# Kernel optimization log

Hardware: AMD Instinct MI355X
Metric: run time of the kernel (lower is better)

## Reference

```python
import jax, jax.numpy as jnp
import numpy as np

FEAT_STRIDE = 8
IM_DIMS = (4096.0, 4096.0)  # (height, width)
ANCHOR_SCALES = (8.0, 16.0, 32.0)
RATIOS = (0.5, 1.0, 2.0)
PRE_NMS_TOPN = 12000   # TRAIN cfg (eval_mode=False)
POST_NMS_TOPN = 2000
NMS_THRESH = 0.7
MIN_SIZE = 16.0


def _generate_anchors(base_size=16.0, ratios=RATIOS, scales=ANCHOR_SCALES):
    ratios = np.array(ratios, np.float32)
    scales = np.array(scales, np.float32)
    w = h = float(base_size)
    x_ctr = 0.5 * (w - 1.0)
    y_ctr = 0.5 * (h - 1.0)
    size = w * h
    ws = np.round(np.sqrt(size / ratios))
    hs = np.round(ws * ratios)
    out = []
    for wr, hr in zip(ws, hs):
        wss = wr * scales
        hss = hr * scales
        out.append(np.stack([x_ctr - 0.5 * (wss - 1.0), y_ctr - 0.5 * (hss - 1.0),
                             x_ctr + 0.5 * (wss - 1.0), y_ctr + 0.5 * (hss - 1.0)], axis=1))
    return np.concatenate(out, 0).astype(np.float32)  # [A=9, 4]


def _nms(boxes, scores, thresh, max_out):
    # greedy sequential NMS; indices are discrete -> stop gradients here
    boxes = jax.lax.stop_gradient(boxes)
    scores = jax.lax.stop_gradient(scores)
    areas = (boxes[:, 2] - boxes[:, 0] + 1.0) * (boxes[:, 3] - boxes[:, 1] + 1.0)

    def body(i, state):
        supp, keep = state
        idx = jnp.argmax(jnp.where(supp, -jnp.inf, scores))
        b = boxes[idx]
        xx1 = jnp.maximum(b[0], boxes[:, 0])
        yy1 = jnp.maximum(b[1], boxes[:, 1])
        xx2 = jnp.minimum(b[2], boxes[:, 2])
        yy2 = jnp.minimum(b[3], boxes[:, 3])
        inter = jnp.maximum(0.0, xx2 - xx1 + 1.0) * jnp.maximum(0.0, yy2 - yy1 + 1.0)
        iou = inter / (areas[idx] + areas - inter)
        supp = supp | (iou > thresh)  # also suppresses idx itself (iou==1)
        keep = keep.at[i].set(idx.astype(jnp.int32))
        return supp, keep

    supp0 = jnp.zeros(boxes.shape[0], dtype=bool)
    keep0 = jnp.zeros(max_out, dtype=jnp.int32)
    _, keep = jax.lax.fori_loop(0, max_out, body, (supp0, keep0))
    return keep


def reference(rpn_cls_score, rpn_bbox_pred):
    _, H, W, C2 = rpn_cls_score.shape
    A = C2 // 2
    # rpn_softmax: per-anchor 2-way (bg, fg) softmax; channels laid out [2, A]
    prob = jax.nn.softmax(rpn_cls_score.reshape(H, W, 2, A), axis=2)
    scores = prob[:, :, 1, :].reshape(-1)           # fg scores, [H*W*A]
    deltas = rpn_bbox_pred.reshape(-1, 4)           # [H*W*A, 4]

    # anchors shifted over the feature grid
    anchors = jnp.asarray(_generate_anchors())       # [A, 4]
    sx = jnp.arange(W, dtype=jnp.float32) * FEAT_STRIDE
    sy = jnp.arange(H, dtype=jnp.float32) * FEAT_STRIDE
    shift_x, shift_y = jnp.meshgrid(sx, sy)          # [H, W]
    shifts = jnp.stack([shift_x, shift_y, shift_x, shift_y], -1).reshape(-1, 1, 4)
    all_anchors = (anchors[None, :, :] + shifts).reshape(-1, 4)  # [H*W*A, 4]

    # bbox_transform_inv
    ws = all_anchors[:, 2] - all_anchors[:, 0] + 1.0
    hs = all_anchors[:, 3] - all_anchors[:, 1] + 1.0
    cx = all_anchors[:, 0] + 0.5 * ws
    cy = all_anchors[:, 1] + 0.5 * hs
    dx, dy, dw, dh = deltas[:, 0], deltas[:, 1], deltas[:, 2], deltas[:, 3]
    pcx = dx * ws + cx
    pcy = dy * hs + cy
    pw = jnp.exp(dw) * ws
    ph = jnp.exp(dh) * hs
    x1 = pcx - 0.5 * pw
    y1 = pcy - 0.5 * ph
    x2 = pcx + 0.5 * pw
    y2 = pcy + 0.5 * ph

    # clip to image boundaries
    x1 = jnp.clip(x1, 0.0, IM_DIMS[1] - 1.0)
    y1 = jnp.clip(y1, 0.0, IM_DIMS[0] - 1.0)
    x2 = jnp.clip(x2, 0.0, IM_DIMS[1] - 1.0)
    y2 = jnp.clip(y2, 0.0, IM_DIMS[0] - 1.0)
    proposals = jnp.stack([x1, y1, x2, y2], axis=1)

    # drop tiny boxes (jit-friendly: -inf score instead of physical removal)
    keep_min = ((x2 - x1 + 1.0) >= MIN_SIZE) & ((y2 - y1 + 1.0) >= MIN_SIZE)
    scores = jnp.where(keep_min, scores, -jnp.inf)

    top_scores, order = jax.lax.top_k(scores, PRE_NMS_TOPN)
    props = proposals[order]                         # [pre_nms_topN, 4]
    keep = _nms(props, top_scores, NMS_THRESH, POST_NMS_TOPN)
    rois = props[keep]                               # [post_nms_topN, 4]
    # blob: [batch_idx(=0), x1, y1, x2, y2]
    return jnp.concatenate([jnp.zeros((POST_NMS_TOPN, 1), rois.dtype), rois], axis=1)


def setup_inputs() -> dict:
    key = jax.random.key(0)
    k1, k2 = jax.random.split(key)
    rpn_cls_score = jax.random.normal(k1, (1, 512, 512, 18), dtype=jnp.float32)
    rpn_bbox_pred = jax.random.normal(k2, (1, 512, 512, 36), dtype=jnp.float32) * 0.2
    return {"rpn_cls_score": rpn_cls_score, "rpn_bbox_pred": rpn_bbox_pred}
```

## Files before the change

kernel.cpp:

```cpp
#include <hip/hip_runtime.h>
#include <cstdint>
#include <cstddef>

#pragma clang fp contract(off)

#define N_ANCH 2359296
#define K_PRE  12000
#define K_POST 2000
#define NWORD  188
#define NC     94
#define TIE_CAP 65536

typedef unsigned int u32;
typedef unsigned long long u64;

__constant__ float c_anch[9][4] = {
  { -84.f,  -40.f,   99.f,   55.f },
  { -176.f, -88.f,  191.f,  103.f },
  { -360.f, -184.f, 375.f,  199.f },
  { -56.f,  -56.f,   71.f,   71.f },
  { -120.f, -120.f, 135.f,  135.f },
  { -248.f, -248.f, 263.f,  263.f },
  { -36.f,  -80.f,   51.f,   95.f },
  { -80.f,  -168.f,  95.f,  183.f },
  { -168.f, -344.f, 183.f,  359.f },
};

__device__ __forceinline__ float pexpf(float xin) {
#pragma clang fp contract(off)
  const float exp_hi = 88.3762626647950f;
  const float exp_lo = -88.3762626647949f;
  const float LOG2EF = 1.44269504088896341f;
  const float C1 = 0.693359375f;
  const float C2 = -2.12194440e-4f;
  const float p0 = 1.9875691500E-4f;
  const float p1 = 1.3981999507E-3f;
  const float p2 = 8.3334519073E-3f;
  const float p3 = 4.1665795894E-2f;
  const float p4 = 1.6666665459E-1f;
  const float p5 = 5.0000001201E-1f;
  float x = fminf(fmaxf(xin, exp_lo), exp_hi);
  float fx = floorf(x * LOG2EF + 0.5f);
  float tmp = C1 * fx;
  float z = C2 * fx;
  x = x - tmp;
  x = x - z;
  z = x * x;
  float y = x * p0 + p1;
  y = y * x + p2;
  y = y * x + p3;
  y = y * x + p4;
  y = y * x + p5;
  y = y * z + x;
  y = 1.0f + y;
  int n = (int)fx;
  u32 e = ((u32)(n + 127)) << 23;
  return y * __uint_as_float(e);
}

__device__ __forceinline__ void decode_box(const float* __restrict__ bbox, int aidx,
                                           float4* ob, float* oarea, bool* okeep) {
#pragma clang fp contract(off)
  int pos = aidx / 9;
  int a = aidx - pos * 9;
  int w = pos & 511;
  int h = pos >> 9;
  float shx = (float)(w * 8);
  float shy = (float)(h * 8);
  float ax1 = c_anch[a][0] + shx;
  float ay1 = c_anch[a][1] + shy;
  float ax2 = c_anch[a][2] + shx;
  float ay2 = c_anch[a][3] + shy;
  float aw = (ax2 - ax1) + 1.0f;
  float ah = (ay2 - ay1) + 1.0f;
  float acx = ax1 + 0.5f * aw;
  float acy = ay1 + 0.5f * ah;
  const float* d = bbox + (size_t)pos * 36 + (size_t)a * 4;
  float dx = d[0], dy = d[1], dw = d[2], dh = d[3];
  float pcx = dx * aw + acx;
  float pcy = dy * ah + acy;
  float pw = pexpf(dw) * aw;
  float ph = pexpf(dh) * ah;
  float x1 = pcx - 0.5f * pw;
  float y1 = pcy - 0.5f * ph;
  float x2 = pcx + 0.5f * pw;
  float y2 = pcy + 0.5f * ph;
  x1 = fminf(fmaxf(x1, 0.0f), 4095.0f);
  y1 = fminf(fmaxf(y1, 0.0f), 4095.0f);
  x2 = fminf(fmaxf(x2, 0.0f), 4095.0f);
  y2 = fminf(fmaxf(y2, 0.0f), 4095.0f);
  *ob = make_float4(x1, y1, x2, y2);
  float ww = (x2 - x1) + 1.0f;
  float hh = (y2 - y1) + 1.0f;
  *oarea = ww * hh;
  *okeep = (ww >= 16.0f) && (hh >= 16.0f);
}

__global__ void k_scores(const float* __restrict__ cls, const float* __restrict__ bbox,
                         u32* __restrict__ keys, u32* __restrict__ ctl,
                         u32* __restrict__ hist) {
#pragma clang fp contract(off)
  int t = blockIdx.x * blockDim.x + threadIdx.x;
  if (blockIdx.x == 0) {
    if (threadIdx.x < 16) ctl[threadIdx.x] = (threadIdx.x == 1) ? (u32)K_PRE : 0u;
    hist[threadIdx.x] = 0u;
  }
  if (t >= N_ANCH) return;
  int pos = t / 9;
  int a = t - pos * 9;
  float s0 = cls[(size_t)pos * 18 + a];
  float s1 = cls[(size_t)pos * 18 + 9 + a];
  float m = fmaxf(s0, s1);
  float e0 = pexpf(s0 - m);
  float e1 = pexpf(s1 - m);
  float p = e1 / (e0 + e1);
  float4 box; float area; bool km;
  decode_box(bbox, t, &box, &area, &km);
  keys[t] = km ? (__float_as_uint(p) | 0x80000000u) : 0u;
}

__global__ void k_histscan(const u32* __restrict__ keys, u32* __restrict__ ctl,
                           u32* __restrict__ hist, int shift, int pass) {
  __shared__ u32 lh[4][256];
  __shared__ u32 s_last;
  int t = threadIdx.x;
  lh[0][t] = 0u; lh[1][t] = 0u; lh[2][t] = 0u; lh[3][t] = 0u;
  __syncthreads();
  int sub = t & 3;
  u32 prefix = ctl[0];
  u32 msk = (shift == 24) ? 0u : (0xFFFFFFFFu << (shift + 8));
  int stride = gridDim.x * blockDim.x;
  for (int i = blockIdx.x * blockDim.x + t; i < N_ANCH; i += stride) {
    u32 k = keys[i];
    if ((k & msk) == prefix) atomicAdd(&lh[sub][(k >> shift) & 0xFFu], 1u);
  }
  __syncthreads();
  u32 hsum = lh[0][t] + lh[1][t] + lh[2][t] + lh[3][t];
  if (hsum) atomicAdd(&hist[t], hsum);
  __syncthreads();
  if (t == 0) {
    __threadfence();
    u32 old = atomicAdd(&ctl[8 + pass], 1u);
    s_last = (old == gridDim.x - 1) ? 1u : 0u;
  }
  __syncthreads();
  if (!s_last) return;
  __threadfence();
  __shared__ u32 sh[256];
  __shared__ u32 horig[256];
  __shared__ int s_d;
  u32 h = atomicAdd(&hist[t], 0u);
  sh[t] = h; horig[t] = h;
  if (t == 0) s_d = 0;
  u32 krem = ctl[1];
  __syncthreads();
  u32 v = h;
  for (int off = 1; off < 256; off <<= 1) {
    u32 add = (t + off < 256) ? sh[t + off] : 0u;
    __syncthreads();
    v += add;
    sh[t] = v;
    __syncthreads();
  }
  if (sh[t] >= krem) atomicMax(&s_d, t);
  __syncthreads();
  if (t == 0) {
    int d = s_d;
    u32 cum = sh[d] - horig[d];
    ctl[0] |= ((u32)d) << shift;
    ctl[1] = krem - cum;
    if (shift == 0) { ctl[2] = ctl[0]; ctl[3] = ctl[1]; }
  }
  hist[t] = 0u;
}

__global__ void k_collect(const u32* __restrict__ keys, u32* __restrict__ ctl,
                          int* __restrict__ sel, int* __restrict__ tie,
                          u64* __restrict__ comps) {
  __shared__ int stI[2048];
  __shared__ u64 stC[2048];
  __shared__ int stT[256];
  __shared__ u32 s_cnt, s_tcnt, s_base, s_tbase;
  int tid = threadIdx.x;
  if (tid == 0) { s_cnt = 0; s_tcnt = 0; }
  __syncthreads();
  u32 kstar = ctl[2];
  int stride = gridDim.x * blockDim.x;
  for (int i = blockIdx.x * blockDim.x + tid; i < N_ANCH; i += stride) {
    u32 k = keys[i];
    if (k > kstar) {
      u32 p = atomicAdd(&s_cnt, 1u);
      u64 cmp = ((u64)k << 32) | (u64)(0xFFFFFFFFu - (u32)i);
      if (p < 2048u) { stI[p] = i; stC[p] = cmp; }
      else { u32 g = atomicAdd(&ctl[4], 1u); sel[g] = i; comps[g] = cmp; }
    } else if (k == kstar) {
      u32 p = atomicAdd(&s_tcnt, 1u);
      if (p < 256u) stT[p] = i;
      else { u32 g = atomicAdd(&ctl[5], 1u); if (g < TIE_CAP) tie[g] = i; }
    }
  }
  __syncthreads();
  if (tid == 0) {
    u32 n = min(s_cnt, 2048u);
    s_base = atomicAdd(&ctl[4], n);
    u32 tn = min(s_tcnt, 256u);
    s_tbase = atomicAdd(&ctl[5], tn);
  }
  __syncthreads();
  u32 n = min(s_cnt, 2048u);
  for (u32 q = tid; q < n; q += blockDim.x) {
    sel[s_base + q] = stI[q];
    comps[s_base + q] = stC[q];
  }
  u32 tn = min(s_tcnt, 256u);
  for (u32 q = tid; q < tn; q += blockDim.x) {
    u32 g = s_tbase + q;
    if (g < TIE_CAP) tie[g] = stT[q];
  }
}

__global__ void k_tiepick(const u32* __restrict__ ctl, const int* __restrict__ tie,
                          int* __restrict__ sel, u64* __restrict__ comps) {
  u32 T = ctl[5]; if (T > TIE_CAP) T = TIE_CAP;
  if (T > 8192u) T = 8192u;
  u32 need = ctl[3];
  u32 base = ctl[4];
  u32 kstar = ctl[2];
  for (u32 t = threadIdx.x; t < T; t += blockDim.x) {
    int v = tie[t];
    u32 r = 0;
    for (u32 u = 0; u < T; ++u) r += (tie[u] < v) ? 1u : 0u;
    if (r < need) {
      sel[base + r] = v;
      comps[base + r] = ((u64)kstar << 32) | (u64)(0xFFFFFFFFu - (u32)v);
    }
  }
}

__global__ void k_rankdec(const u64* __restrict__ comps, const int* __restrict__ sel,
                          const float* __restrict__ bbox,
                          float4* __restrict__ props, float* __restrict__ areas) {
  __shared__ u64 tile[2048];
  int tid = threadIdx.x;
  int lane = tid & 63;
  int wave = tid >> 6;
  int base = (blockIdx.x * 4 + wave) * 8;
  u64 c0 = comps[base + 0], c1 = comps[base + 1], c2 = comps[base + 2], c3 = comps[base + 3];
  u64 c4 = comps[base + 4], c5 = comps[base + 5], c6 = comps[base + 6], c7 = comps[base + 7];
  int n0 = 0, n1 = 0, n2 = 0, n3 = 0, n4 = 0, n5 = 0, n6 = 0, n7 = 0;
  for (int t0 = 0; t0 < K_PRE; t0 += 2048) {
    int cnt = min(2048, K_PRE - t0);
    __syncthreads();
    for (int q = tid; q < cnt; q += 256) tile[q] = comps[t0 + q];
    __syncthreads();
    for (int q = lane; q < cnt; q += 64) {
      u64 v = tile[q];
      n0 += (v > c0); n1 += (v > c1); n2 += (v > c2); n3 += (v > c3);
      n4 += (v > c4); n5 += (v > c5); n6 += (v > c6); n7 += (v > c7);
    }
  }
  for (int off = 32; off; off >>= 1) {
    n0 += __shfl_xor(n0, off); n1 += __shfl_xor(n1, off);
    n2 += __shfl_xor(n2, off); n3 += __shfl_xor(n3, off);
    n4 += __shfl_xor(n4, off); n5 += __shfl_xor(n5, off);
    n6 += __shfl_xor(n6, off); n7 += __shfl_xor(n7, off);
  }
  int rk = n0;
  rk = (lane == 1) ? n1 : rk; rk = (lane == 2) ? n2 : rk;
  rk = (lane == 3) ? n3 : rk; rk = (lane == 4) ? n4 : rk;
  rk = (lane == 5) ? n5 : rk; rk = (lane == 6) ? n6 : rk;
  rk = (lane == 7) ? n7 : rk;
  if (lane < 8) {
    float4 box; float area; bool km;
    decode_box(bbox, sel[base + lane], &box, &area, &km);
    props[rk] = box;
    areas[rk] = area;
  }
}

__device__ __forceinline__ int d2idx(int c, int h, int lane) {
  return ((c * 2 + h) * 64 + lane) * 2;
}

__global__ void k_mask(const float4* __restrict__ props, const float* __restrict__ areas,
                       u64* __restrict__ mask, u64* __restrict__ diag2,
                       u64* __restrict__ sub2) {
#pragma clang fp contract(off)
  int x = blockIdx.x, y = blockIdx.y;
  int cx = x >> 1, cy = y >> 1;
  if (cy + 1 < cx || cy == cx + 1) return;
  __shared__ float4 bj[64];
  __shared__ float aj[64];
  int j0 = y * 64;
  bj[threadIdx.x] = props[j0 + threadIdx.x];
  aj[threadIdx.x] = areas[j0 + threadIdx.x];
  __syncthreads();
  int i = x * 64 + threadIdx.x;
  float4 bi = props[i];
  float ai = areas[i];
  u64 bits = 0;
  for (int jj = 0; jj < 64; ++jj) {
    int j = j0 + jj;
    float4 bb = bj[jj];
    float xx1 = fmaxf(bi.x, bb.x);
    float yy1 = fmaxf(bi.y, bb.y);
    float xx2 = fminf(bi.z, bb.z);
    float yy2 = fminf(bi.w, bb.w);
    float w = fmaxf(0.0f, (xx2 - xx1) + 1.0f);
    float h = fmaxf(0.0f, (yy2 - yy1) + 1.0f);
    float inter = w * h;
    float iou = inter / ((ai + aj[jj]) - inter);
    if ((iou > 0.7f) && (j < K_PRE)) bits |= (1ull << jj);
  }
  if (cy == cx)          diag2[d2idx(cx, x & 1, threadIdx.x) + (y & 1)] = bits;
  else if (cy == cx - 1) sub2[d2idx(cx, x & 1, threadIdx.x) + (y & 1)] = bits;
  else                   mask[(size_t)i * NWORD + y] = bits;
}

#define NMS_BAR() asm volatile("s_waitcnt lgkmcnt(0)\n\ts_barrier" ::: "memory")

typedef __attribute__((address_space(1))) const u32* gas_p;
typedef __attribute__((address_space(3))) u32* las_p;
__device__ __forceinline__ void gll16(const u64* g, u64* l) {
  __builtin_amdgcn_global_load_lds((gas_p)g, (las_p)l, 16, 0, 0);
}

__global__ void __launch_bounds__(1024, 1) k_nms(const u64* __restrict__ mask,
                                                 const u64* __restrict__ diag2,
                                                 const u64* __restrict__ sub2,
                                                 const float4* __restrict__ props,
                                                 float* __restrict__ out) {
  __shared__ u64 rem[NWORD];
  __shared__ int keepb[K_POST];
  __shared__ int kept[2][128];
  __shared__ u64 dstage[2][2][64][2];
  __shared__ u64 sstage[2][2][64][2];
  __shared__ int s_kk[2];
  __shared__ int s_nk;
  __shared__ int s_brk;
  int tid = threadIdx.x;
  int lane = tid & 63;
  int wave = tid >> 6;
  for (int w = tid; w < NWORD; w += 1024) {
    int base = w * 64;
    u64 v;
    if (base + 64 <= K_PRE) v = 0ull;
    else if (base >= K_PRE) v = ~0ull;
    else v = (~0ull) << (K_PRE - base);
    rem[w] = v;
  }
  if (tid == 0) { s_nk = 0; s_brk = 0; s_kk[0] = 0; s_kk[1] = 0; }
  if (wave == 0) {
    gll16(diag2 + d2idx(0, 0, lane), &dstage[0][0][0][0]);
    gll16(diag2 + d2idx(0, 1, lane), &dstage[0][1][0][0]);
    gll16(sub2 + d2idx(1, 0, lane), &sstage[1][0][0][0]);
    gll16(sub2 + d2idx(1, 1, lane), &sstage[1][1][0][0]);
  }
  __syncthreads();

  int nk = 0;

  for (int c = 0; c < NC; ++c) {
    if (s_brk) break;
    int par = c & 1;
    if (wave == 0) {
      int cn = min(c + 1, NC - 1);
      int cs = min(c + 2, NC - 1);
      gll16(diag2 + d2idx(cn, 0, lane), &dstage[cn & 1][0][0][0]);
      gll16(diag2 + d2idx(cn, 1, lane), &dstage[cn & 1][1][0][0]);
      gll16(sub2 + d2idx(cs, 0, lane), &sstage[cs & 1][0][0][0]);
      gll16(sub2 + d2idx(cs, 1, lane), &sstage[cs & 1][1][0][0]);
      asm volatile("s_waitcnt vmcnt(4)" ::: "memory");
      u64 dl0A = dstage[par][0][lane][0], dl1A = dstage[par][0][lane][1];
      u64 dh0A = dstage[par][1][lane][0], dh1A = dstage[par][1][lane][1];
      int ps = (c + 1) & 1;
      u64 sl0A = sstage[ps][0][lane][0], sl1A = sstage[ps][0][lane][1];
      u64 sh0A = sstage[ps][1][lane][0], sh1A = sstage[ps][1][lane][1];
      u64 w0 = ~rem[2 * c];
      u64 w1 = ~rem[2 * c + 1];
      u64 km0 = 0, km1 = 0;
      int nk0 = nk;
      while (w0 != 0ull && nk < K_POST) {
        int j = (int)__builtin_ctzll(w0);
        u64 sup = __ballot((int)((dl0A >> j) & 1ull));
        km0 |= (1ull << j);
        nk++;
        w0 &= ~sup;
      }
      if (km0) w1 &= ~__ballot((int)((dh0A & km0) != 0ull));
      while (w1 != 0ull && nk < K_POST) {
        int j = (int)__builtin_ctzll(w1);
        u64 sup = __ballot((int)((dh1A >> j) & 1ull));
        km1 |= (1ull << j);
        nk++;
        w1 &= ~sup;
      }
      int ncnt0 = __popcll(km0);
      u64 below = (1ull << lane) - 1ull;
      if ((km0 >> lane) & 1ull) {
        int pos = nk0 + __popcll(km0 & below);
        int idx = (c << 7) | lane;
        keepb[pos] = idx;
        kept[par][pos - nk0] = idx;
      }
      if ((km1 >> lane) & 1ull) {
        int pos = nk0 + ncnt0 + __popcll(km1 & below);
        int idx = (c << 7) | 64 | lane;
        keepb[pos] = idx;
        kept[par][pos - nk0] = idx;
      }
      if (c + 1 < NC) {
        int plo = (int)((((sl0A & km0) | (sl1A & km1)) != 0ull) ? 1 : 0);
        int phi = (int)((((sh0A & km0) | (sh1A & km1)) != 0ull) ? 1 : 0);
        u64 vlo = __ballot(plo);
        u64 vhi = __ballot(phi);
        if (lane == 0) {
          if (vlo) atomicOr((unsigned long long*)&rem[2 * c + 2], (unsigned long long)vlo);
          if (vhi) atomicOr((unsigned long long*)&rem[2 * c + 3], (unsigned long long)vhi);
        }
      }
      if (lane == 0) { s_kk[par] = nk - nk0; s_nk = nk; s_brk = (nk >= K_POST) ? 1 : 0; }
    } else if (c >= 1) {
      int kkp = s_kk[par ^ 1];
      const int* kb = &kept[par ^ 1][0];
      int wv = wave - 1;
      int seg = wv % 3;
      int q0 = wv / 3;
      int w = 2 * c + 2 + seg * 64 + lane;
      if (kkp > q0 && w < NWORD) {
        int m = kkp - 1;
        int i0 = kb[q0];
        int i1 = kb[min(q0 + 5, m)];
        int i2 = kb[min(q0 + 10, m)];
        int i3 = kb[min(q0 + 15, m)];
        int i4 = kb[min(q0 + 20, m)];
        int i5 = kb[min(q0 + 25, m)];
        int i6 = kb[min(q0 + 30, m)];
        int i7 = kb[min(q0 + 35, m)];
        u64 fp0 = mask[(size_t)i0 * NWORD + w];
        u64 fp1 = mask[(size_t)i1 * NWORD + w];
        u64 fp2 = mask[(size_t)i2 * NWORD + w];
        u64 fp3 = mask[(size_t)i3 * NWORD + w];
        u64 fp4 = mask[(size_t)i4 * NWORD + w];
        u64 fp5 = mask[(size_t)i5 * NWORD + w];
        u64 fp6 = mask[(size_t)i6 * NWORD + w];
        u64 fp7 = mask[(size_t)i7 * NWORD + w];
        u64 v = (fp0 | fp1) | (fp2 | fp3) | ((fp4 | fp5) | (fp6 | fp7));
        for (int q = q0 + 40; q < kkp; q += 5)
          v |= mask[(size_t)kb[q] * NWORD + w];
        if (v) atomicOr((unsigned long long*)&rem[w], (unsigned long long)v);
      }
    }
    NMS_BAR();
  }
  __syncthreads();
  int fnk = s_nk;
  for (int t = tid; t < K_POST; t += 1024) {
    int kidx = (t < fnk) ? keepb[t] : 0;
    float4 b = props[kidx];
    out[t * 5 + 0] = 0.0f;
    out[t * 5 + 1] = b.x;
    out[t * 5 + 2] = b.y;
    out[t * 5 + 3] = b.z;
    out[t * 5 + 4] = b.w;
  }
}

extern "C" void kernel_launch(void* const* d_in, const int* in_sizes, int n_in,
                              void* d_out, int out_size, void* d_ws, size_t ws_size,
                              hipStream_t stream) {
  const float* cls  = (const float*)d_in[0];
  const float* bbox = (const float*)d_in[1];
  float* out = (float*)d_out;
  char* ws = (char*)d_ws;

  u64* mask    = (u64*)ws;
  u32* keys    = (u32*)ws;
  u32* ctl     = (u32*)(ws + 9437184);
  u32* hist    = (u32*)(ws + 9437248);
  int* sel     = (int*)(ws + 9438464);
  int* tie     = (int*)(ws + 9486592);
  u64* comps   = (u64*)(ws + 18096128);
  float4* props= (float4*)(ws + 18240512);
  float* areas = (float*)(ws + 18433024);
  u64* diag2   = (u64*)(ws + 18481152);
  u64* sub2    = (u64*)(ws + 18673664);

  k_scores<<<dim3((N_ANCH + 255) / 256), dim3(256), 0, stream>>>(cls, bbox, keys, ctl, hist);
  const int shifts[4] = {24, 16, 8, 0};
  for (int s = 0; s < 4; ++s)
    k_histscan<<<dim3(256), dim3(256), 0, stream>>>(keys, ctl, hist, shifts[s], s);
  k_collect<<<dim3(256), dim3(256), 0, stream>>>(keys, ctl, sel, tie, comps);
  k_tiepick<<<dim3(1), dim3(256), 0, stream>>>(ctl, tie, sel, comps);
  k_rankdec<<<dim3(375), dim3(256), 0, stream>>>(comps, sel, bbox, props, areas);
  k_mask<<<dim3(188, 188), dim3(64), 0, stream>>>(props, areas, mask, diag2, sub2);
  k_nms<<<dim3(1), dim3(1024), 0, stream>>>(mask, diag2, sub2, props, out);
}
```

Measured before the change: 319.3 us.

## Widen histogram/collect blocks to 1024 threads and batch NMS mask loads via inline asm

The radix-select histogram and collect kernels now launch 1024-thread blocks instead of 256, with guards so that only the first 256 threads handle per-bin work. This adds more in-flight loads during the full scans over the keys. In the NMS kernel, the eight gathered mask loads are issued back-to-back in inline assembly with a single wait, forcing memory-level parallelism. The inline asm blocks compiler scheduling, and the shared staging buffers in k_collect may behave differently with four times the threads per block.

Result: faster. 304.8 us, median of 2 (-4.6%).

```diff
diff --git a/kernel.cpp b/kernel.cpp
--- a/kernel.cpp
+++ b/kernel.cpp
@@ -103,7 +103,7 @@
   int t = blockIdx.x * blockDim.x + threadIdx.x;
   if (blockIdx.x == 0) {
     if (threadIdx.x < 16) ctl[threadIdx.x] = (threadIdx.x == 1) ? (u32)K_PRE : 0u;
-    hist[threadIdx.x] = 0u;
+    if (threadIdx.x < 256) hist[threadIdx.x] = 0u;
   }
   if (t >= N_ANCH) return;
   int pos = t / 9;
@@ -119,12 +119,14 @@
   keys[t] = km ? (__float_as_uint(p) | 0x80000000u) : 0u;
 }
 
-__global__ void k_histscan(const u32* __restrict__ keys, u32* __restrict__ ctl,
-                           u32* __restrict__ hist, int shift, int pass) {
+__global__ void __launch_bounds__(1024) k_histscan(const u32* __restrict__ keys,
+                                                   u32* __restrict__ ctl,
+                                                   u32* __restrict__ hist,
+                                                   int shift, int pass) {
   __shared__ u32 lh[4][256];
   __shared__ u32 s_last;
   int t = threadIdx.x;
-  lh[0][t] = 0u; lh[1][t] = 0u; lh[2][t] = 0u; lh[3][t] = 0u;
+  if (t < 256) { lh[0][t] = 0u; lh[1][t] = 0u; lh[2][t] = 0u; lh[3][t] = 0u; }
   __syncthreads();
   int sub = t & 3;
   u32 prefix = ctl[0];
@@ -135,8 +137,10 @@
     if ((k & msk) == prefix) atomicAdd(&lh[sub][(k >> shift) & 0xFFu], 1u);
   }
   __syncthreads();
-  u32 hsum = lh[0][t] + lh[1][t] + lh[2][t] + lh[3][t];
-  if (hsum) atomicAdd(&hist[t], hsum);
+  if (t < 256) {
+    u32 hsum = lh[0][t] + lh[1][t] + lh[2][t] + lh[3][t];
+    if (hsum) atomicAdd(&hist[t], hsum);
+  }
   __syncthreads();
   if (t == 0) {
     __threadfence();
@@ -149,20 +153,22 @@
   __shared__ u32 sh[256];
   __shared__ u32 horig[256];
   __shared__ int s_d;
-  u32 h = atomicAdd(&hist[t], 0u);
-  sh[t] = h; horig[t] = h;
+  u32 h = 0;
+  if (t < 256) {
+    h = atomicAdd(&hist[t], 0u);
+    sh[t] = h; horig[t] = h;
+  }
   if (t == 0) s_d = 0;
   u32 krem = ctl[1];
   __syncthreads();
   u32 v = h;
   for (int off = 1; off < 256; off <<= 1) {
-    u32 add = (t + off < 256) ? sh[t + off] : 0u;
+    u32 add = (t < 256 && t + off < 256) ? sh[t + off] : 0u;
     __syncthreads();
-    v += add;
-    sh[t] = v;
+    if (t < 256) { v += add; sh[t] = v; }
     __syncthreads();
   }
-  if (sh[t] >= krem) atomicMax(&s_d, t);
+  if (t < 256 && sh[t] >= krem) atomicMax(&s_d, t);
   __syncthreads();
   if (t == 0) {
     int d = s_d;
@@ -171,12 +177,14 @@
     ctl[1] = krem - cum;
     if (shift == 0) { ctl[2] = ctl[0]; ctl[3] = ctl[1]; }
   }
-  hist[t] = 0u;
-}
-
-__global__ void k_collect(const u32* __restrict__ keys, u32* __restrict__ ctl,
-                          int* __restrict__ sel, int* __restrict__ tie,
-                          u64* __restrict__ comps) {
+  if (t < 256) hist[t] = 0u;
+}
+
+__global__ void __launch_bounds__(1024) k_collect(const u32* __restrict__ keys,
+                                                  u32* __restrict__ ctl,
+                                                  int* __restrict__ sel,
+                                                  int* __restrict__ tie,
+                                                  u64* __restrict__ comps) {
   __shared__ int stI[2048];
   __shared__ u64 stC[2048];
   __shared__ int stT[256];
@@ -429,22 +437,30 @@
       int w = 2 * c + 2 + seg * 64 + lane;
       if (kkp > q0 && w < NWORD) {
         int m = kkp - 1;
-        int i0 = kb[q0];
-        int i1 = kb[min(q0 + 5, m)];
-        int i2 = kb[min(q0 + 10, m)];
-        int i3 = kb[min(q0 + 15, m)];
-        int i4 = kb[min(q0 + 20, m)];
-        int i5 = kb[min(q0 + 25, m)];
-        int i6 = kb[min(q0 + 30, m)];
-        int i7 = kb[min(q0 + 35, m)];
-        u64 fp0 = mask[(size_t)i0 * NWORD + w];
-        u64 fp1 = mask[(size_t)i1 * NWORD + w];
-        u64 fp2 = mask[(size_t)i2 * NWORD + w];
-        u64 fp3 = mask[(size_t)i3 * NWORD + w];
-        u64 fp4 = mask[(size_t)i4 * NWORD + w];
-        u64 fp5 = mask[(size_t)i5 * NWORD + w];
-        u64 fp6 = mask[(size_t)i6 * NWORD + w];
-        u64 fp7 = mask[(size_t)i7 * NWORD + w];
+        const u64* p0 = mask + (size_t)kb[q0] * NWORD + w;
+        const u64* p1 = mask + (size_t)kb[min(q0 + 5, m)] * NWORD + w;
+        const u64* p2 = mask + (size_t)kb[min(q0 + 10, m)] * NWORD + w;
+        const u64* p3 = mask + (size_t)kb[min(q0 + 15, m)] * NWORD + w;
+        const u64* p4 = mask + (size_t)kb[min(q0 + 20, m)] * NWORD + w;
+        const u64* p5 = mask + (size_t)kb[min(q0 + 25, m)] * NWORD + w;
+        const u64* p6 = mask + (size_t)kb[min(q0 + 30, m)] * NWORD + w;
+        const u64* p7 = mask + (size_t)kb[min(q0 + 35, m)] * NWORD + w;
+        u64 fp0, fp1, fp2, fp3, fp4, fp5, fp6, fp7;
+        asm volatile(
+          "global_load_dwordx2 %0, %8, off\n\t"
+          "global_load_dwordx2 %1, %9, off\n\t"
+          "global_load_dwordx2 %2, %10, off\n\t"
+          "global_load_dwordx2 %3, %11, off\n\t"
+          "global_load_dwordx2 %4, %12, off\n\t"
+          "global_load_dwordx2 %5, %13, off\n\t"
+          "global_load_dwordx2 %6, %14, off\n\t"
+          "global_load_dwordx2 %7, %15, off\n\t"
+          "s_waitcnt vmcnt(0)"
+          : "=&v"(fp0), "=&v"(fp1), "=&v"(fp2), "=&v"(fp3),
+            "=&v"(fp4), "=&v"(fp5), "=&v"(fp6), "=&v"(fp7)
+          : "v"(p0), "v"(p1), "v"(p2), "v"(p3),
+            "v"(p4), "v"(p5), "v"(p6), "v"(p7)
+          : "memory");
         u64 v = (fp0 | fp1) | (fp2 | fp3) | ((fp4 | fp5) | (fp6 | fp7));
         for (int q = q0 + 40; q < kkp; q += 5)
           v |= mask[(size_t)kb[q] * NWORD + w];
@@ -489,8 +505,8 @@
   k_scores<<<dim3((N_ANCH + 255) / 256), dim3(256), 0, stream>>>(cls, bbox, keys, ctl, hist);
   const int shifts[4] = {24, 16, 8, 0};
   for (int s = 0; s < 4; ++s)
-    k_histscan<<<dim3(256), dim3(256), 0, stream>>>(keys, ctl, hist, shifts[s], s);
-  k_collect<<<dim3(256), dim3(256), 0, stream>>>(keys, ctl, sel, tie, comps);
+    k_histscan<<<dim3(256), dim3(1024), 0, stream>>>(keys, ctl, hist, shifts[s], s);
+  k_collect<<<dim3(256), dim3(1024), 0, stream>>>(keys, ctl, sel, tie, comps);
   k_tiepick<<<dim3(1), dim3(256), 0, stream>>>(ctl, tie, sel, comps);
   k_rankdec<<<dim3(375), dim3(256), 0, stream>>>(comps, sel, bbox, props, areas);
   k_mask<<<dim3(188, 188), dim3(64), 0, stream>>>(props, areas, mask, diag2, sub2);
```
